# Kernel tuning notes

Hardware: AMD Instinct MI355X
Metric: run time of the kernel (lower is better)

Reference implementation:

```python
import jax, jax.numpy as jnp
import numpy as np
from jax import lax

HUMAN_SIZE = 54
NUM_ACTIONS = 1
INPUT_SIZE = HUMAN_SIZE + NUM_ACTIONS  # 55, one_hot=True
RNN_SIZE = 1024
SOURCE_SEQ_LEN = 50
TARGET_SEQ_LEN = 25
BATCH = 1024


def setup_inputs() -> dict:
    key = jax.random.key(0)
    ks = jax.random.split(key, 8)
    s = 1.0 / np.sqrt(RNN_SIZE)
    return {
        "encoder_inputs": jax.random.normal(ks[0], (BATCH, SOURCE_SEQ_LEN, INPUT_SIZE), jnp.float32),
        "decoder_inputs": jax.random.normal(ks[1], (BATCH, TARGET_SEQ_LEN, INPUT_SIZE), jnp.float32),
        "W_ih": jax.random.uniform(ks[2], (3 * RNN_SIZE, INPUT_SIZE), jnp.float32, -s, s),
        "W_hh": jax.random.uniform(ks[3], (3 * RNN_SIZE, RNN_SIZE), jnp.float32, -s, s),
        "b_ih": jax.random.uniform(ks[4], (3 * RNN_SIZE,), jnp.float32, -s, s),
        "b_hh": jax.random.uniform(ks[5], (3 * RNN_SIZE,), jnp.float32, -s, s),
        "fc_w": jax.random.uniform(ks[6], (INPUT_SIZE, RNN_SIZE), jnp.float32, -s, s),
        "fc_b": jax.random.uniform(ks[7], (INPUT_SIZE,), jnp.float32, -s, s),
    }


def _gru_step(h, x, W_ih, W_hh, b_ih, b_hh):
    # torch.nn.GRUCell math
    gi = x @ W_ih.T + b_ih            # [B, 3H]
    gh = h @ W_hh.T + b_hh            # [B, 3H]
    i_r, i_z, i_n = jnp.split(gi, 3, axis=-1)
    h_r, h_z, h_n = jnp.split(gh, 3, axis=-1)
    r = jax.nn.sigmoid(i_r + h_r)
    z = jax.nn.sigmoid(i_z + h_z)
    n = jnp.tanh(i_n + r * h_n)
    return (1.0 - z) * n + z * h


def reference(encoder_inputs, decoder_inputs, W_ih, W_hh, b_ih, b_hh, fc_w, fc_b):
    B = encoder_inputs.shape[0]
    H = W_hh.shape[1]
    state0 = jnp.zeros((B, H), dtype=encoder_inputs.dtype)

    # Encoder: first source_seq_len-1 frames, time-major scan (dropout p=0 -> identity)
    enc_tm = jnp.swapaxes(encoder_inputs[:, : SOURCE_SEQ_LEN - 1], 0, 1)  # [S-1, B, In]

    def enc_step(h, x):
        return _gru_step(h, x, W_ih, W_hh, b_ih, b_hh), None

    state, _ = lax.scan(enc_step, state0, enc_tm)

    def dec_step(carry, _):
        h, inp = carry
        inp = lax.stop_gradient(inp)  # inp.detach()
        h = _gru_step(h, inp, W_ih, W_hh, b_ih, b_hh)
        out = inp + h @ fc_w.T + fc_b  # residual add
        return (h, out), out

    (_, _), outs = lax.scan(dec_step, (state, decoder_inputs[:, 0]), None, length=TARGET_SEQ_LEN)
    return jnp.swapaxes(outs, 0, 1)  # [B, T, In]
```

## Files before the change

kernel.cpp:

```cpp
#include <hip/hip_runtime.h>


typedef unsigned short ushort_t;
typedef __bf16 bf16x8 __attribute__((ext_vector_type(8)));
typedef float f32x4 __attribute__((ext_vector_type(4)));
typedef unsigned int u32x4 __attribute__((ext_vector_type(4)));

#define MFMA(a, b, c) __builtin_amdgcn_mfma_f32_16x16x32_bf16(a, b, c, 0, 0, 0)

static __device__ __forceinline__ ushort_t f2bf(float f) {
  union { float f; unsigned u; } x; x.f = f;
  unsigned r = x.u + 0x7fffu + ((x.u >> 16) & 1u);
  return (ushort_t)(r >> 16);
}
static __device__ __forceinline__ float sigmf(float x) { return 1.f / (1.f + __expf(-x)); }
static __device__ __forceinline__ float tanhf_(float x) { return 1.f - 2.f / (__expf(2.f * x) + 1.f); }

static __device__ __forceinline__ __amdgpu_buffer_rsrc_t mkrsrc(const void* p) {
  return __builtin_amdgcn_make_buffer_rsrc(const_cast<void*>(p), (short)0, -1, 0x00020000);
}
#if __has_builtin(__builtin_amdgcn_raw_buffer_load_b128)
static __device__ __forceinline__ bf16x8 ldb(__amdgpu_buffer_rsrc_t r, int voff) {
  u32x4 v = __builtin_amdgcn_raw_buffer_load_b128(r, voff, 0, 1);
  union { u32x4 u; bf16x8 b; } x; x.u = v; return x.b;
}
static __device__ __forceinline__ bf16x8 ldbc(__amdgpu_buffer_rsrc_t r, int voff) {
  u32x4 v = __builtin_amdgcn_raw_buffer_load_b128(r, voff, 0, 0);
  union { u32x4 u; bf16x8 b; } x; x.u = v; return x.b;
}
#else
static __device__ __forceinline__ bf16x8 ldb(__amdgpu_buffer_rsrc_t r, int voff) {
  union { unsigned u[4]; bf16x8 b; } x;
  x.u[0] = __builtin_amdgcn_raw_buffer_load_b32(r, voff, 0, 1);
  x.u[1] = __builtin_amdgcn_raw_buffer_load_b32(r, voff + 4, 0, 1);
  x.u[2] = __builtin_amdgcn_raw_buffer_load_b32(r, voff + 8, 0, 1);
  x.u[3] = __builtin_amdgcn_raw_buffer_load_b32(r, voff + 12, 0, 1);
  return x.b;
}
static __device__ __forceinline__ bf16x8 ldbc(__amdgpu_buffer_rsrc_t r, int voff) {
  union { unsigned u[4]; bf16x8 b; } x;
  x.u[0] = __builtin_amdgcn_raw_buffer_load_b32(r, voff, 0, 0);
  x.u[1] = __builtin_amdgcn_raw_buffer_load_b32(r, voff + 4, 0, 0);
  x.u[2] = __builtin_amdgcn_raw_buffer_load_b32(r, voff + 8, 0, 0);
  x.u[3] = __builtin_amdgcn_raw_buffer_load_b32(r, voff + 12, 0, 0);
  return x.b;
}
#endif

__global__ __launch_bounds__(512, 2)
void seq2seq_xcd(const float* __restrict__ enc, const float* __restrict__ dec,
                 const float* __restrict__ Wih, const float* __restrict__ Whh,
                 const float* __restrict__ b_ih, const float* __restrict__ b_hh,
                 const float* __restrict__ fcw, const float* __restrict__ fcb,
                 float* __restrict__ outp,
                 ushort_t* __restrict__ xg, ushort_t* __restrict__ hA,
                 ushort_t* __restrict__ innA, ushort_t* __restrict__ nG,
                 ushort_t* __restrict__ fcG, unsigned* cnt) {
  __shared__ ushort_t WrzL[65536];
  __shared__ ushort_t WiL[6144];
  __shared__ float scratchF[4096];
  __shared__ unsigned sgs;

  const int tid = threadIdx.x;
  const int w = tid >> 6, l = tid & 63;
  const int fr = l & 15, fq4 = l >> 4;

  if (tid == 0) {
    unsigned x;
    asm volatile("s_getreg_b32 %0, hwreg(HW_REG_XCC_ID, 0, 8)" : "=s"(x));
    x &= 7u;
    unsigned s = atomicAdd(&cnt[x * 64], 1u);
    sgs = (x << 8) | s;
  }
  __syncthreads();
  const int g = sgs >> 8, slot = sgs & 255;
  const bool isFC = (slot >= 24);

  unsigned* arrp = cnt + (8 + g) * 64;
  auto fcpp = [&](int td) { return cnt + (48 + g * 25 + td) * 64; };

  ushort_t* hbase = hA + (size_t)g * 262144;
  auto hb = [&](int i) { return hbase + (size_t)i * 131072; };
  ushort_t* xgg = xg + (size_t)g * 49 * 8192;
  auto inng = [&](int i) { return innA + (size_t)(g * 2 + i) * 8192; };
  ushort_t* nGp = nG + (size_t)(g * 32 + slot) * 32768;
  ushort_t* fcGg = fcG + (size_t)g * 65536;

  for (int i = tid; i < 65536; i += 512) {
    int j = i & 7, ln = (i >> 3) & 63, jf = (i >> 9) & 1, gt = (i >> 10) & 1, kt = i >> 11;
    int col = gt * 1024 + slot * 32 + jf * 16 + (ln & 15);
    int k = kt * 32 + (ln >> 4) * 8 + j;
    WrzL[i] = f2bf(Whh[(size_t)col * 1024 + k]);
  }
  for (int i = tid; i < 6144; i += 512) {
    int j = i & 7, ln = (i >> 3) & 63, jf = (i >> 9) & 1, rem = i >> 10;
    int gt = rem % 3, kt = rem / 3;
    int col = gt * 1024 + slot * 32 + jf * 16 + (ln & 15);
    int k = kt * 32 + (ln >> 4) * 8 + j;
    WiL[i] = (k < 55) ? f2bf(Wih[(size_t)col * 55 + k]) : (ushort_t)0;
  }
  for (int i = tid; i < 32768; i += 512) {
    int j = i & 7, ln = (i >> 3) & 63, jf = (i >> 9) & 1, kt = i >> 10;
    int col = 2048 + slot * 32 + jf * 16 + (ln & 15);
    int k = kt * 32 + (ln >> 4) * 8 + j;
    nGp[i] = f2bf(Whh[(size_t)col * 1024 + k]);
  }
#pragma unroll
  for (int rep = 0; rep < 2; ++rep) {
    int t = slot + rep * 32;
    if (t < 49) {
      ushort_t* xp = xgg + (size_t)t * 8192;
      for (int i = tid; i < 8192; i += 512) {
        int sub = i & 7, row = (i >> 3) & 127, kc = i >> 10;
        int c = kc * 8 + sub;
        xp[i] = (c < 55) ? f2bf(enc[((size_t)(g * 128 + row) * 50 + t) * 55 + c]) : (ushort_t)0;
      }
    }
  }
  if (slot < 4) {
    ushort_t* ip = inng(0);
    for (int i = slot * 2048 + tid; i < (slot + 1) * 2048; i += 512) {
      int sub = i & 7, row = (i >> 3) & 127, kc = i >> 10;
      int c = kc * 8 + sub;
      ip[i] = (c < 55) ? f2bf(dec[(size_t)(g * 128 + row) * 1375 + c]) : (ushort_t)0;
    }
  }
  if (isFC) {
    for (int i = (slot - 24) * 8192 + tid; i < (slot - 23) * 8192; i += 512) {
      int j = i & 7, ln = (i >> 3) & 63, jf = (i >> 9) & 3, kt = i >> 11;
      int c = jf * 16 + (ln & 15);
      int k = kt * 32 + (ln >> 4) * 8 + j;
      fcGg[i] = (c < 55) ? f2bf(fcw[(size_t)c * 1024 + k]) : (ushort_t)0;
    }
  }

  float brz[2], bzz[2], bin[2], bhn[2];
#pragma unroll
  for (int jf = 0; jf < 2; ++jf) {
    int col = slot * 32 + jf * 16 + fr;
    brz[jf] = b_ih[col] + b_hh[col];
    bzz[jf] = b_ih[1024 + col] + b_hh[1024 + col];
    bin[jf] = b_ih[2048 + col];
    bhn[jf] = b_hh[2048 + col];
  }
  const int Rfc = (slot - 24) * 16;
  const int jfF = w & 3;
  const int colF = jfF * 16 + fr;
  float fcbF = 0.f, inp[4] = {0.f, 0.f, 0.f, 0.f};
  if (isFC && w < 4) {
    fcbF = (colF < 55) ? fcb[colF] : 0.f;
#pragma unroll
    for (int v = 0; v < 4; ++v)
      inp[v] = (colF < 55) ? dec[(size_t)(g * 128 + Rfc + fq4 * 4 + v) * 1375 + colF] : 0.f;
  }
  f32x4 hreg0 = (f32x4){0.f, 0.f, 0.f, 0.f};
  f32x4 hreg1 = (f32x4){0.f, 0.f, 0.f, 0.f};

  auto arrive = [&](unsigned k) {
    (void)k;
    __syncthreads();
    if (tid == 0) atomicAdd(arrp, 1u);
  };
  auto wait_rel = [&](unsigned k) {
    if (tid == 0) {
      while (__hip_atomic_load(arrp, __ATOMIC_RELAXED, __HIP_MEMORY_SCOPE_AGENT) < 32u * k)
        __builtin_amdgcn_s_sleep(1);
    }
    __syncthreads();
  };
  auto fc_wait = [&](int td) {
    if (tid == 0) {
      while (__hip_atomic_load(fcpp(td), __ATOMIC_RELAXED, __HIP_MEMORY_SCOPE_AGENT) < 8u)
        __builtin_amdgcn_s_sleep(1);
    }
    __syncthreads();
  };

  f32x4 av[12], nx0, nx1;

  auto xpart = [&](const ushort_t* xp) {
    __amdgpu_buffer_rsrc_t rx = mkrsrc(xp);
    const int R = (w & 3) * 32 + (w >> 2) * 16;
#pragma unroll
    for (int kt = 0; kt < 2; ++kt) {
      bf16x8 a = ldb(rx, ((kt * 4 + fq4) * 128 + R + fr) * 16);
      const ushort_t* bl = WiL + kt * 3072 + l * 8;
      bf16x8 br_0 = *(const bf16x8*)(bl);
      bf16x8 br_1 = *(const bf16x8*)(bl + 512);
      bf16x8 bz_0 = *(const bf16x8*)(bl + 1024);
      bf16x8 bz_1 = *(const bf16x8*)(bl + 1536);
      bf16x8 bn_0 = *(const bf16x8*)(bl + 2048);
      bf16x8 bn_1 = *(const bf16x8*)(bl + 2560);
      if (w < 4) {
        av[0] = MFMA(a, br_0, av[0]);
        av[1] = MFMA(a, br_1, av[1]);
        av[4] = MFMA(a, bz_0, av[4]);
        av[5] = MFMA(a, bz_1, av[5]);
      } else {
        av[2] = MFMA(a, br_0, av[2]);
        av[3] = MFMA(a, br_1, av[3]);
        av[6] = MFMA(a, bz_0, av[6]);
        av[7] = MFMA(a, bz_1, av[7]);
      }
      nx0 = MFMA(a, bn_0, nx0);
      nx1 = MFMA(a, bn_1, nx1);
    }
  };

  auto hpart = [&](const ushort_t* hbp) {
    __amdgpu_buffer_rsrc_t r = mkrsrc(hbp);
    __amdgpu_buffer_rsrc_t rn = mkrsrc(nGp);
    const int kh = w >> 2, R = (w & 3) * 32;
    bf16x8 A0[4], A1[4];
    bf16x8 NG[4][2];
#pragma unroll
    for (int i = 0; i < 4; ++i) {
      int kt = kh * 16 + i;
      A0[i] = ldb(r, ((kt * 4 + fq4) * 128 + R + fr) * 16);
      A1[i] = ldb(r, ((kt * 4 + fq4) * 128 + R + 16 + fr) * 16);
      NG[i][0] = ldbc(rn, kt * 2048 + l * 16);
      NG[i][1] = ldbc(rn, kt * 2048 + 1024 + l * 16);
    }
    const ushort_t* bl0 = WrzL + (kh * 16) * 2048 + l * 8;
    bf16x8 br0 = *(const bf16x8*)(bl0);
    bf16x8 br1 = *(const bf16x8*)(bl0 + 512);
    bf16x8 bz0 = *(const bf16x8*)(bl0 + 1024);
    bf16x8 bz1 = *(const bf16x8*)(bl0 + 1536);
#pragma unroll
    for (int i = 0; i < 16; ++i) {
      int kt = kh * 16 + i;
      bf16x8 a0 = A0[i & 3], a1 = A1[i & 3];
      bf16x8 n0 = NG[i & 3][0], n1 = NG[i & 3][1];
      bf16x8 cr0 = br0, cr1 = br1, cz0 = bz0, cz1 = bz1;
      if (i < 15) {
        const ushort_t* bln = WrzL + (kt + 1) * 2048 + l * 8;
        br0 = *(const bf16x8*)(bln);
        br1 = *(const bf16x8*)(bln + 512);
        bz0 = *(const bf16x8*)(bln + 1024);
        bz1 = *(const bf16x8*)(bln + 1536);
      }
      if (i < 12) {
        int kp = kt + 4;
        A0[i & 3] = ldb(r, ((kp * 4 + fq4) * 128 + R + fr) * 16);
        A1[i & 3] = ldb(r, ((kp * 4 + fq4) * 128 + R + 16 + fr) * 16);
        NG[i & 3][0] = ldbc(rn, kp * 2048 + l * 16);
        NG[i & 3][1] = ldbc(rn, kp * 2048 + 1024 + l * 16);
      }
      av[0] = MFMA(a0, cr0, av[0]);
      av[2] = MFMA(a1, cr0, av[2]);
      av[1] = MFMA(a0, cr1, av[1]);
      av[3] = MFMA(a1, cr1, av[3]);
      av[4] = MFMA(a0, cz0, av[4]);
      av[6] = MFMA(a1, cz0, av[6]);
      av[5] = MFMA(a0, cz1, av[5]);
      av[7] = MFMA(a1, cz1, av[7]);
      av[8] = MFMA(a0, n0, av[8]);
      av[10] = MFMA(a1, n0, av[10]);
      av[9] = MFMA(a0, n1, av[9]);
      av[11] = MFMA(a1, n1, av[11]);
    }
  };

#define KXCH(LO0, LO1, HI0, HI1)                                    \
  do {                                                              \
    if (w >= 4) {                                                   \
      float* sp_ = scratchF + ((w - 4) * 64 + l) * 4;               \
      *(f32x4*)(sp_) = av[LO0];                                     \
      *(f32x4*)(sp_ + 1024) = av[LO1];                              \
    } else {                                                        \
      float* sp_ = scratchF + (w * 64 + l) * 4;                     \
      *(f32x4*)(sp_ + 2048) = av[HI0];                              \
      *(f32x4*)(sp_ + 3072) = av[HI1];                              \
    }                                                               \
    __syncthreads();                                                \
    if (w < 4) {                                                    \
      const float* sp_ = scratchF + (w * 64 + l) * 4;               \
      av[LO0] += *(const f32x4*)(sp_);                              \
      av[LO1] += *(const f32x4*)(sp_ + 1024);                       \
    } else {                                                        \
      const float* sp_ = scratchF + ((w - 4) * 64 + l) * 4;         \
      av[HI0] += *(const f32x4*)(sp_ + 2048);                       \
      av[HI1] += *(const f32x4*)(sp_ + 3072);                       \
    }                                                               \
    __syncthreads();                                                \
  } while (0)

#define EPI(RV, ZV, NHV, NXV, JF, HC)                                  \
  do {                                                                 \
    const int kq_ = slot * 4 + (JF)*2 + (fr >> 3);                     \
    _Pragma("unroll") for (int v = 0; v < 4; ++v) {                    \
      float rr = sigmf(RV[v] + brz[JF]);                               \
      float zz = sigmf(ZV[v] + bzz[JF]);                               \
      float nn = tanhf_(NXV[v] + bin[JF] + rr * (NHV[v] + bhn[JF]));   \
      float h = (1.f - zz) * nn + zz * HC[v];                          \
      HC[v] = h;                                                       \
      int row_ = Rbase + fq4 * 4 + v;                                  \
      hn[(kq_ * 128 + row_) * 8 + sub_] = f2bf(h);                     \
    }                                                                  \
  } while (0)

  auto fcdo = [&](const ushort_t* hbp, int td, bool wr, ushort_t* innW) {
    __amdgpu_buffer_rsrc_t r = mkrsrc(hbp);
    __amdgpu_buffer_rsrc_t rf = mkrsrc(fcGg);
    const int kh = w >> 2;
    f32x4 fa = (f32x4){0.f, 0.f, 0.f, 0.f};
    bf16x8 Af[4], Bf[4];
#pragma unroll
    for (int i = 0; i < 4; ++i) {
      int kt = kh * 16 + i;
      Af[i] = ldb(r, ((kt * 4 + fq4) * 128 + Rfc + fr) * 16);
      Bf[i] = ldbc(rf, (kt * 4 + jfF) * 1024 + l * 16);
    }
#pragma unroll
    for (int i = 0; i < 16; ++i) {
      int kt = kh * 16 + i;
      bf16x8 a = Af[i & 3], bb = Bf[i & 3];
      if (i < 12) {
        Af[i & 3] = ldb(r, (((kt + 4) * 4 + fq4) * 128 + Rfc + fr) * 16);
        Bf[i & 3] = ldbc(rf, ((kt + 4) * 4 + jfF) * 1024 + l * 16);
      }
      fa = MFMA(a, bb, fa);
    }
    if (w >= 4) *(f32x4*)(scratchF + ((w - 4) * 64 + l) * 4) = fa;
    __syncthreads();
    if (w < 4) {
      fa += *(const f32x4*)(scratchF + (w * 64 + l) * 4);
      const int kq = colF >> 3, sub = colF & 7;
#pragma unroll
      for (int v = 0; v < 4; ++v) {
        int row = Rfc + fq4 * 4 + v;
        float o = fa[v] + inp[v] + fcbF;
        inp[v] = o;
        if (wr) innW[(kq * 128 + row) * 8 + sub] = f2bf(o);
        if (colF < 55) outp[(size_t)(g * 128 + row) * 1375 + td * 55 + colF] = o;
      }
    }
    __syncthreads();
  };

  arrive(1);
  wait_rel(1);

  for (int t = 0; t < 74; ++t) {
#pragma unroll
    for (int i = 0; i < 12; ++i) av[i] = (f32x4){0.f, 0.f, 0.f, 0.f};
    nx0 = (f32x4){0.f, 0.f, 0.f, 0.f};
    nx1 = (f32x4){0.f, 0.f, 0.f, 0.f};

    if (t <= 49) {
      xpart(t <= 48 ? xgg + (size_t)t * 8192 : inng(0));
    }
    if (t > 0) wait_rel(t + 1);
    if (t >= 50 && isFC) {
      fcdo(hb(t & 1), t - 50, true, inng((t - 49) & 1));
      if (tid == 0) atomicAdd(fcpp(t - 50), 1u);
    }
    if (t > 0) hpart(hb(t & 1));
    if (t >= 50) {
      fc_wait(t - 50);
      xpart(inng((t - 49) & 1));
    }
    KXCH(0, 1, 2, 3);
    KXCH(4, 5, 6, 7);
    KXCH(8, 9, 10, 11);
    {
      ushort_t* hn = hb((t + 1) & 1);
      const int Rbase = (w & 3) * 32 + (w >> 2) * 16;
      const int sub_ = fr & 7;
      if (w < 4) {
        EPI(av[0], av[4], av[8], nx0, 0, hreg0);
        EPI(av[1], av[5], av[9], nx1, 1, hreg1);
      } else {
        EPI(av[2], av[6], av[10], nx0, 0, hreg0);
        EPI(av[3], av[7], av[11], nx1, 1, hreg1);
      }
    }
    arrive(t + 2);
  }

  if (isFC) {
    wait_rel(75);
    fcdo(hb(0), 24, false, (ushort_t*)0);
  }
}

extern "C" void kernel_launch(void* const* d_in, const int* in_sizes, int n_in,
                              void* d_out, int out_size, void* d_ws, size_t ws_size,
                              hipStream_t stream) {
  const float* enc  = (const float*)d_in[0];
  const float* dec  = (const float*)d_in[1];
  const float* Wih  = (const float*)d_in[2];
  const float* Whh  = (const float*)d_in[3];
  const float* b_ih = (const float*)d_in[4];
  const float* b_hh = (const float*)d_in[5];
  const float* fcw  = (const float*)d_in[6];
  const float* fcb  = (const float*)d_in[7];
  float* out = (float*)d_out;

  char* ws = (char*)d_ws;
  unsigned* cnt  = (unsigned*)ws; ws += 65536;
  ushort_t* xg   = (ushort_t*)ws; ws += (size_t)8 * 49 * 8192 * 2;
  ushort_t* hA   = (ushort_t*)ws; ws += (size_t)8 * 2 * 131072 * 2;
  ushort_t* innA = (ushort_t*)ws; ws += (size_t)8 * 2 * 8192 * 2;
  ushort_t* nG   = (ushort_t*)ws; ws += (size_t)8 * 32 * 32768 * 2;
  ushort_t* fcG  = (ushort_t*)ws; ws += (size_t)8 * 65536 * 2;

  (void)hipMemsetAsync(cnt, 0, 65536, stream);
  seq2seq_xcd<<<256, 512, 0, stream>>>(
      enc, dec, Wih, Whh, b_ih, b_hh, fcw, fcb, out,
      xg, hA, innA, nG, fcG, cnt);
}
```

Before: 794.0 us.

## Shard barrier counters, prefetch weights before wait, drop trailing exchange sync

The per-group arrival counter is split into four counters indexed by slot, and waiters sum all four, which is meant to reduce atomic contention on a single cache line. The loads of the n-gate weights and the first W_hh rz fragments are issued before the grid-barrier wait, so their latency hides behind the spin. The final __syncthreads after the last K-exchange is removed, relying on the epilogue and the arrive barrier for ordering. The cost is extra register pressure from the prefetched fragments, four loads per spin iteration, and a possible LDS reuse hazard if the removed sync was needed.

After: 781.6 us. No clear change (-1.6%).

```diff
diff --git a/kernel.cpp b/kernel.cpp
--- a/kernel.cpp
+++ b/kernel.cpp
@@ -76,7 +76,8 @@
   const int g = sgs >> 8, slot = sgs & 255;
   const bool isFC = (slot >= 24);
 
-  unsigned* arrp = cnt + (8 + g) * 64;
+  unsigned* arr4 = cnt + (8 + g * 4 + (slot & 3)) * 64;
+  unsigned* arrb = cnt + (8 + g * 4) * 64;
   auto fcpp = [&](int td) { return cnt + (48 + g * 25 + td) * 64; };
 
   ushort_t* hbase = hA + (size_t)g * 262144;
@@ -156,15 +157,20 @@
   f32x4 hreg0 = (f32x4){0.f, 0.f, 0.f, 0.f};
   f32x4 hreg1 = (f32x4){0.f, 0.f, 0.f, 0.f};
 
-  auto arrive = [&](unsigned k) {
-    (void)k;
+  auto arrive = [&]() {
     __syncthreads();
-    if (tid == 0) atomicAdd(arrp, 1u);
+    if (tid == 0) atomicAdd(arr4, 1u);
   };
   auto wait_rel = [&](unsigned k) {
     if (tid == 0) {
-      while (__hip_atomic_load(arrp, __ATOMIC_RELAXED, __HIP_MEMORY_SCOPE_AGENT) < 32u * k)
+      for (;;) {
+        unsigned s0 = __hip_atomic_load(arrb, __ATOMIC_RELAXED, __HIP_MEMORY_SCOPE_AGENT);
+        unsigned s1 = __hip_atomic_load(arrb + 64, __ATOMIC_RELAXED, __HIP_MEMORY_SCOPE_AGENT);
+        unsigned s2 = __hip_atomic_load(arrb + 128, __ATOMIC_RELAXED, __HIP_MEMORY_SCOPE_AGENT);
+        unsigned s3 = __hip_atomic_load(arrb + 192, __ATOMIC_RELAXED, __HIP_MEMORY_SCOPE_AGENT);
+        if (s0 + s1 + s2 + s3 >= 32u * k) break;
         __builtin_amdgcn_s_sleep(1);
+      }
     }
     __syncthreads();
   };
@@ -177,6 +183,11 @@
   };
 
   f32x4 av[12], nx0, nx1;
+  bf16x8 pA0[4], pA1[4];
+  bf16x8 pN0[4], pN1[4];
+  bf16x8 pb0, pb1, pb2, pb3;
+
+  __amdgpu_buffer_rsrc_t rnG = mkrsrc(nGp);
 
   auto xpart = [&](const ushort_t* xp) {
     __amdgpu_buffer_rsrc_t rx = mkrsrc(xp);
@@ -207,30 +218,36 @@
     }
   };
 
-  auto hpart = [&](const ushort_t* hbp) {
-    __amdgpu_buffer_rsrc_t r = mkrsrc(hbp);
-    __amdgpu_buffer_rsrc_t rn = mkrsrc(nGp);
-    const int kh = w >> 2, R = (w & 3) * 32;
-    bf16x8 A0[4], A1[4];
-    bf16x8 NG[4][2];
+  auto hpre = [&]() {
+    const int kh = w >> 2;
 #pragma unroll
     for (int i = 0; i < 4; ++i) {
       int kt = kh * 16 + i;
-      A0[i] = ldb(r, ((kt * 4 + fq4) * 128 + R + fr) * 16);
-      A1[i] = ldb(r, ((kt * 4 + fq4) * 128 + R + 16 + fr) * 16);
-      NG[i][0] = ldbc(rn, kt * 2048 + l * 16);
-      NG[i][1] = ldbc(rn, kt * 2048 + 1024 + l * 16);
+      pN0[i] = ldbc(rnG, kt * 2048 + l * 16);
+      pN1[i] = ldbc(rnG, kt * 2048 + 1024 + l * 16);
     }
     const ushort_t* bl0 = WrzL + (kh * 16) * 2048 + l * 8;
-    bf16x8 br0 = *(const bf16x8*)(bl0);
-    bf16x8 br1 = *(const bf16x8*)(bl0 + 512);
-    bf16x8 bz0 = *(const bf16x8*)(bl0 + 1024);
-    bf16x8 bz1 = *(const bf16x8*)(bl0 + 1536);
+    pb0 = *(const bf16x8*)(bl0);
+    pb1 = *(const bf16x8*)(bl0 + 512);
+    pb2 = *(const bf16x8*)(bl0 + 1024);
+    pb3 = *(const bf16x8*)(bl0 + 1536);
+  };
+
+  auto hmain = [&](const ushort_t* hbp) {
+    __amdgpu_buffer_rsrc_t r = mkrsrc(hbp);
+    const int kh = w >> 2, R = (w & 3) * 32;
+#pragma unroll
+    for (int i = 0; i < 4; ++i) {
+      int kt = kh * 16 + i;
+      pA0[i] = ldb(r, ((kt * 4 + fq4) * 128 + R + fr) * 16);
+      pA1[i] = ldb(r, ((kt * 4 + fq4) * 128 + R + 16 + fr) * 16);
+    }
+    bf16x8 br0 = pb0, br1 = pb1, bz0 = pb2, bz1 = pb3;
 #pragma unroll
     for (int i = 0; i < 16; ++i) {
       int kt = kh * 16 + i;
-      bf16x8 a0 = A0[i & 3], a1 = A1[i & 3];
-      bf16x8 n0 = NG[i & 3][0], n1 = NG[i & 3][1];
+      bf16x8 a0 = pA0[i & 3], a1 = pA1[i & 3];
+      bf16x8 n0 = pN0[i & 3], n1 = pN1[i & 3];
       bf16x8 cr0 = br0, cr1 = br1, cz0 = bz0, cz1 = bz1;
       if (i < 15) {
         const ushort_t* bln = WrzL + (kt + 1) * 2048 + l * 8;
@@ -241,10 +258,10 @@
       }
       if (i < 12) {
         int kp = kt + 4;
-        A0[i & 3] = ldb(r, ((kp * 4 + fq4) * 128 + R + fr) * 16);
-        A1[i & 3] = ldb(r, ((kp * 4 + fq4) * 128 + R + 16 + fr) * 16);
-        NG[i & 3][0] = ldbc(rn, kp * 2048 + l * 16);
-        NG[i & 3][1] = ldbc(rn, kp * 2048 + 1024 + l * 16);
+        pA0[i & 3] = ldb(r, ((kp * 4 + fq4) * 128 + R + fr) * 16);
+        pA1[i & 3] = ldb(r, ((kp * 4 + fq4) * 128 + R + 16 + fr) * 16);
+        pN0[i & 3] = ldbc(rnG, kp * 2048 + l * 16);
+        pN1[i & 3] = ldbc(rnG, kp * 2048 + 1024 + l * 16);
       }
       av[0] = MFMA(a0, cr0, av[0]);
       av[2] = MFMA(a1, cr0, av[2]);
@@ -261,7 +278,7 @@
     }
   };
 
-#define KXCH(LO0, LO1, HI0, HI1)                                    \
+#define KXCH(LO0, LO1, HI0, HI1, TS)                                \
   do {                                                              \
     if (w >= 4) {                                                   \
       float* sp_ = scratchF + ((w - 4) * 64 + l) * 4;               \
@@ -282,7 +299,7 @@
       av[HI0] += *(const f32x4*)(sp_ + 2048);                       \
       av[HI1] += *(const f32x4*)(sp_ + 3072);                       \
     }                                                               \
-    __syncthreads();                                                \
+    if (TS) __syncthreads();                                        \
   } while (0)
 
 #define EPI(RV, ZV, NHV, NXV, JF, HC)                                  \
@@ -338,7 +355,7 @@
     __syncthreads();
   };
 
-  arrive(1);
+  arrive();
   wait_rel(1);
 
   for (int t = 0; t < 74; ++t) {
@@ -350,19 +367,22 @@
     if (t <= 49) {
       xpart(t <= 48 ? xgg + (size_t)t * 8192 : inng(0));
     }
-    if (t > 0) wait_rel(t + 1);
+    if (t > 0) {
+      hpre();
+      wait_rel(t + 1);
+    }
     if (t >= 50 && isFC) {
       fcdo(hb(t & 1), t - 50, true, inng((t - 49) & 1));
       if (tid == 0) atomicAdd(fcpp(t - 50), 1u);
     }
-    if (t > 0) hpart(hb(t & 1));
+    if (t > 0) hmain(hb(t & 1));
     if (t >= 50) {
       fc_wait(t - 50);
       xpart(inng((t - 49) & 1));
     }
-    KXCH(0, 1, 2, 3);
-    KXCH(4, 5, 6, 7);
-    KXCH(8, 9, 10, 11);
+    KXCH(0, 1, 2, 3, 1);
+    KXCH(4, 5, 6, 7, 1);
+    KXCH(8, 9, 10, 11, 0);
     {
       ushort_t* hn = hb((t + 1) & 1);
       const int Rbase = (w & 3) * 32 + (w >> 2) * 16;
@@ -375,7 +395,7 @@
         EPI(av[3], av[7], av[11], nx1, 1, hreg1);
       }
     }
-    arrive(t + 2);
+    arrive();
   }
 
   if (isFC) {
```
